# Kernel optimization log

Measured on AMD Instinct MI355X. Metric: run time of the kernel, lower is better.

Reference implementation:

```python
import jax, jax.numpy as jnp
import numpy as np

DECAY = 0.8
CODEBOOK_SIZE = 1024
DIM = 128


def setup_inputs() -> dict:
    key = jax.random.key(0)
    k1, k2 = jax.random.split(key)
    x = jax.random.normal(k1, (16, 4096, DIM), dtype=jnp.float32)
    embed = jax.random.normal(k2, (CODEBOOK_SIZE, DIM), dtype=jnp.float32)
    ema_embed = embed * 1.0  # ema_num_initial = 1.0
    ema_num = jnp.ones((CODEBOOK_SIZE,), dtype=jnp.float32)
    return {"x": x, "embed": embed, "ema_embed": ema_embed, "ema_num": ema_num}


def reference(x, embed, ema_embed, ema_num):
    # flatten: [..., d] -> [N, d]
    shape = x.shape
    flatten = x.reshape(-1, shape[-1])  # [N, d]
    distance = -2.0 * (flatten @ embed.T) + jnp.sum(embed * embed, axis=-1)  # [N, K]
    embed_ind = jnp.argmin(distance, axis=-1)  # [N]
    quantize = embed[embed_ind.reshape(shape[:-1])]  # gather -> [..., d]

    # training branch: onehot^T @ flatten == segment_sum over code indices
    num_curr = jax.ops.segment_sum(
        jnp.ones_like(embed_ind, dtype=jnp.float32), embed_ind,
        num_segments=CODEBOOK_SIZE)  # [K]
    embed_curr = jax.ops.segment_sum(
        flatten.astype(jnp.float32), embed_ind,
        num_segments=CODEBOOK_SIZE)  # [K, d]

    ema_num_new = ema_num * DECAY + (1.0 - DECAY) * num_curr
    ema_embed_new = ema_embed * DECAY + (1.0 - DECAY) * embed_curr
    embed_new = ema_embed_new / ema_num_new[:, None]
    return quantize, embed_new, ema_embed_new, ema_num_new
```

## Files before the change

kernel.cpp:

```cpp
#include <hip/hip_runtime.h>

#define NPTS   65536
#define DIM    128
#define KCODES 1024
#define BM     128
#define TILE_C 32
#define NTHR   256
#define HALF_C 512

typedef short bf16x8 __attribute__((ext_vector_type(8)));
typedef float f32x4  __attribute__((ext_vector_type(4)));

__device__ __forceinline__ short f2bf(float f) {
    unsigned u = __builtin_bit_cast(unsigned, f);
    u = (u + 0x7fffu + ((u >> 16) & 1u)) >> 16;
    return (short)u;
}
__device__ __forceinline__ float bf2f(short s) {
    unsigned u = ((unsigned)(unsigned short)s) << 16;
    return __builtin_bit_cast(float, u);
}
__device__ __forceinline__ void gload_lds16(const void* g, void* l) {
    __builtin_amdgcn_global_load_lds(
        (const __attribute__((address_space(1))) void*)g,
        (__attribute__((address_space(3))) void*)l, 16, 0, 0);
}

__global__ __launch_bounds__(256)
void pack_kernel(const float* __restrict__ embed, short* __restrict__ ebf,
                 int* __restrict__ ghist, int* __restrict__ gcursor,
                 const float* __restrict__ ema_embed,
                 float* __restrict__ acc, float* __restrict__ hn)
{
    __shared__ float partial[256];
    const int t   = threadIdx.x;
    const int b   = blockIdx.x;
    const int g   = b * 256 + t;
    if (g < KCODES) { ghist[g] = 0; gcursor[g] = 0; }
    {
        float4 e = reinterpret_cast<const float4*>(ema_embed)[g];
        float4 o = {0.8f * e.x, 0.8f * e.y, 0.8f * e.z, 0.8f * e.w};
        reinterpret_cast<float4*>(acc)[g] = o;
    }
    const int tc  = g >> 10;
    const int f   = (g >> 6) & 15;
    const int l   = g & 63;
    const int h   = f >> 3;
    const int nt  = (f >> 2) & 1;
    const int akk = f & 3;
    const int hg  = l >> 4;
    const int n   = l & 15;
    const int c   = tc * TILE_C + nt * 16 + n;
    const int d0  = akk * 32 + hg * 8;
    const float* src = embed + (long)c * DIM + d0;
    float4 v0 = *reinterpret_cast<const float4*>(src);
    float4 v1 = *reinterpret_cast<const float4*>(src + 4);
    float vv[8] = {v0.x, v0.y, v0.z, v0.w, v1.x, v1.y, v1.z, v1.w};
    bf16x8 out;
    float ss = 0.f;
    #pragma unroll
    for (int j = 0; j < 8; ++j) {
        short hi = f2bf(vv[j]);
        out[j] = h ? f2bf(vv[j] - bf2f(hi)) : hi;
        ss += vv[j] * vv[j];
    }
    *reinterpret_cast<bf16x8*>(ebf + (long)g * 8) = out;

    if (h == 0) {
        partial[t] = ss;
        __syncthreads();
        if (t < 16) {
            float s = 0.f;
            #pragma unroll
            for (int k = 0; k < 16; ++k) s += partial[t + k * 16];
            hn[tc * TILE_C + nt * 16 + t] = 0.5f * s;
        }
    }
}

__global__ __launch_bounds__(NTHR, 2)
void argmin_kernel(const float* __restrict__ x, const short* __restrict__ ebf,
                   const float* __restrict__ halfnorm, float2* __restrict__ bvbi)
{
    __shared__ short es[2][8192];

    const int t    = threadIdx.x;
    const int lane = t & 63;
    const int w    = t >> 6;
    const int r16  = lane & 15;
    const int h4   = lane >> 4;
    const int half = blockIdx.y;
    const long xbase = (long)blockIdx.x * BM * DIM;
    const int  wp    = w * 32;
    const long sbase = (long)half * 16 * 8192;
    const int  cbase = half * HALF_C;

    bf16x8 ahi[2][4], alo[2][4];
    #pragma unroll
    for (int ms = 0; ms < 2; ++ms) {
        const long prow = xbase + (long)(wp + ms * 16 + r16) * DIM;
        #pragma unroll
        for (int kk = 0; kk < 4; ++kk) {
            const float* s = x + prow + kk * 32 + h4 * 8;
            float4 u0 = *reinterpret_cast<const float4*>(s);
            float4 u1 = *reinterpret_cast<const float4*>(s + 4);
            float vv[8] = {u0.x, u0.y, u0.z, u0.w, u1.x, u1.y, u1.z, u1.w};
            #pragma unroll
            for (int j = 0; j < 8; ++j) {
                short hi = f2bf(vv[j]);
                ahi[ms][kk][j] = hi;
                alo[ms][kk][j] = f2bf(vv[j] - bf2f(hi));
            }
        }
    }

    #pragma unroll
    for (int i = 0; i < 4; ++i) {
        const int f = w * 4 + i;
        gload_lds16(ebf + sbase + f * 512 + lane * 8, &es[0][f * 512]);
    }
    float hnv_cur[2];
    #pragma unroll
    for (int nt = 0; nt < 2; ++nt) hnv_cur[nt] = halfnorm[cbase + nt * 16 + r16];
    __syncthreads();

    float bestv[8];
    int   besti[8];
    #pragma unroll
    for (int s = 0; s < 8; ++s) { bestv[s] = -1e30f; besti[s] = 0; }

    for (int tile = 0; tile < HALF_C / TILE_C; ++tile) {
        float hnv_nxt[2] = {0.f, 0.f};
        if (tile + 1 < HALF_C / TILE_C) {
            const long gbase = sbase + (long)(tile + 1) * 8192;
            #pragma unroll
            for (int i = 0; i < 4; ++i) {
                const int f = w * 4 + i;
                gload_lds16(ebf + gbase + f * 512 + lane * 8, &es[(tile + 1) & 1][f * 512]);
            }
            #pragma unroll
            for (int nt = 0; nt < 2; ++nt)
                hnv_nxt[nt] = halfnorm[cbase + (tile + 1) * TILE_C + nt * 16 + r16];
        }

        const short* buf = es[tile & 1];
        f32x4 C[2][2];
        #pragma unroll
        for (int nt = 0; nt < 2; ++nt)
            #pragma unroll
            for (int ms = 0; ms < 2; ++ms) C[nt][ms] = (f32x4){0.f, 0.f, 0.f, 0.f};

        #pragma unroll
        for (int akk = 0; akk < 4; ++akk) {
            #pragma unroll
            for (int nt = 0; nt < 2; ++nt) {
                bf16x8 Bh = *reinterpret_cast<const bf16x8*>(buf + (nt * 4 + akk) * 512 + lane * 8);
                bf16x8 Bl = *reinterpret_cast<const bf16x8*>(buf + (8 + nt * 4 + akk) * 512 + lane * 8);
                C[nt][0] = __builtin_amdgcn_mfma_f32_16x16x32_bf16(ahi[0][akk], Bh, C[nt][0], 0, 0, 0);
                C[nt][1] = __builtin_amdgcn_mfma_f32_16x16x32_bf16(ahi[1][akk], Bh, C[nt][1], 0, 0, 0);
                C[nt][0] = __builtin_amdgcn_mfma_f32_16x16x32_bf16(alo[0][akk], Bh, C[nt][0], 0, 0, 0);
                C[nt][1] = __builtin_amdgcn_mfma_f32_16x16x32_bf16(alo[1][akk], Bh, C[nt][1], 0, 0, 0);
                C[nt][0] = __builtin_amdgcn_mfma_f32_16x16x32_bf16(ahi[0][akk], Bl, C[nt][0], 0, 0, 0);
                C[nt][1] = __builtin_amdgcn_mfma_f32_16x16x32_bf16(ahi[1][akk], Bl, C[nt][1], 0, 0, 0);
            }
        }

        #pragma unroll
        for (int nt = 0; nt < 2; ++nt) {
            const int c = cbase + tile * TILE_C + nt * 16 + r16;
            #pragma unroll
            for (int ms = 0; ms < 2; ++ms)
                #pragma unroll
                for (int reg = 0; reg < 4; ++reg) {
                    float sc  = C[nt][ms][reg] - hnv_cur[nt];
                    int  slot = ms * 4 + reg;
                    if (sc > bestv[slot]) { bestv[slot] = sc; besti[slot] = c; }
                }
        }
        hnv_cur[0] = hnv_nxt[0];
        hnv_cur[1] = hnv_nxt[1];
        __syncthreads();
    }

    #pragma unroll
    for (int s = 0; s < 8; ++s) {
        float v = bestv[s];
        int   i = besti[s];
        #pragma unroll
        for (int off = 1; off < 16; off <<= 1) {
            float ov = __shfl_xor(v, off);
            int   oi = __shfl_xor(i, off);
            if (ov > v || (ov == v && oi < i)) { v = ov; i = oi; }
        }
        bestv[s] = v; besti[s] = i;
    }
    if (r16 == 0) {
        #pragma unroll
        for (int s = 0; s < 8; ++s) {
            int ms = s >> 2, reg = s & 3;
            int p  = wp + ms * 16 + h4 * 4 + reg;
            bvbi[(long)half * NPTS + blockIdx.x * BM + p] =
                (float2){bestv[s], __int_as_float(besti[s])};
        }
    }
}

__global__ __launch_bounds__(256)
void merge_kernel(const float2* __restrict__ bvbi, const float* __restrict__ embed,
                  int* __restrict__ ind, float* __restrict__ quant,
                  int* __restrict__ ghist)
{
    __shared__ int hist[KCODES];
    __shared__ int bidx[256];
    const int t    = threadIdx.x;
    const int base = blockIdx.x * 256;

    for (int i = t; i < KCODES; i += 256) hist[i] = 0;

    float2 a = bvbi[base + t];
    float2 b = bvbi[NPTS + base + t];
    const int best = (a.x >= b.x) ? __float_as_int(a.y) : __float_as_int(b.y);
    bidx[t] = best;
    ind[base + t] = best;
    __syncthreads();
    atomicAdd(&hist[best], 1);
    __syncthreads();
    for (int i = t; i < KCODES; i += 256)
        if (hist[i]) atomicAdd(&ghist[i], hist[i]);

    float4* dst = reinterpret_cast<float4*>(quant + (long)base * DIM);
    #pragma unroll
    for (int i = 0; i < 32; ++i) {
        int idx = i * 256 + t;
        int p   = idx >> 5;
        int q   = idx & 31;
        int c   = bidx[p];
        dst[idx] = reinterpret_cast<const float4*>(embed + (long)c * DIM)[q];
    }
}

__global__ __launch_bounds__(256)
void scatter_kernel(const int* __restrict__ ghist, const int* __restrict__ ind,
                    const float* __restrict__ ema_num, float* __restrict__ ema_num_new,
                    int* __restrict__ gcursor, int* __restrict__ sorted,
                    int* __restrict__ scode)
{
    __shared__ int off_lds[KCODES];
    __shared__ int wsum[4];
    const int t    = threadIdx.x;
    const int lane = t & 63;
    const int w    = t >> 6;

    int v[4], pre[4];
    int s = 0;
    #pragma unroll
    for (int j = 0; j < 4; ++j) {
        v[j] = ghist[t * 4 + j];
        pre[j] = s;
        s += v[j];
    }
    int incl = s;
    #pragma unroll
    for (int off = 1; off < 64; off <<= 1) {
        int u = __shfl_up(incl, off);
        if (lane >= off) incl += u;
    }
    if (lane == 63) wsum[w] = incl;
    __syncthreads();
    if (t == 0) {
        int a = 0;
        #pragma unroll
        for (int k = 0; k < 4; ++k) { int tmp = wsum[k]; wsum[k] = a; a += tmp; }
    }
    __syncthreads();
    const int excl = wsum[w] + incl - s;
    #pragma unroll
    for (int j = 0; j < 4; ++j) off_lds[t * 4 + j] = excl + pre[j];

    if (blockIdx.x == 0) {
        #pragma unroll
        for (int j = 0; j < 4; ++j)
            ema_num_new[t * 4 + j] = ema_num[t * 4 + j] * 0.8f + 0.2f * (float)v[j];
    }
    __syncthreads();

    const int p = blockIdx.x * 256 + t;
    const int c = ind[p];
    const int pos = off_lds[c] + atomicAdd(&gcursor[c], 1);
    sorted[pos] = p;
    scode[pos]  = c;
}

__global__ __launch_bounds__(128)
void sum2_kernel(const float* __restrict__ x, const int* __restrict__ sorted,
                 const int* __restrict__ scode, float* __restrict__ acc)
{
    __shared__ int sp[64];
    __shared__ int sc[64];
    const int t = threadIdx.x;
    const int base = blockIdx.x * 64;
    if (t < 64) { sp[t] = sorted[base + t]; sc[t] = scode[base + t]; }
    __syncthreads();

    float a = 0.f;
    int cprev = sc[0];
    #pragma unroll 1
    for (int kk = 0; kk < 8; ++kk) {
        float v[8];
        #pragma unroll
        for (int i = 0; i < 8; ++i)
            v[i] = x[(long)sp[kk * 8 + i] * DIM + t];
        #pragma unroll
        for (int i = 0; i < 8; ++i) {
            const int c = sc[kk * 8 + i];
            if (c != cprev) {
                atomicAdd(&acc[(long)cprev * DIM + t], 0.2f * a);
                a = 0.f; cprev = c;
            }
            a += v[i];
        }
    }
    atomicAdd(&acc[(long)cprev * DIM + t], 0.2f * a);
}

__global__ __launch_bounds__(256)
void final_kernel(const float* __restrict__ acc, const float* __restrict__ ema_num_new,
                  float* __restrict__ embed_new)
{
    const int g = blockIdx.x * 256 + threadIdx.x;
    float4 v = reinterpret_cast<const float4*>(acc)[g];
    const float en = ema_num_new[g >> 5];
    float4 o = {v.x / en, v.y / en, v.z / en, v.w / en};
    reinterpret_cast<float4*>(embed_new)[g] = o;
}

extern "C" void kernel_launch(void* const* d_in, const int* in_sizes, int n_in,
                              void* d_out, int out_size, void* d_ws, size_t ws_size,
                              hipStream_t stream)
{
    const float* x         = (const float*)d_in[0];
    const float* embed     = (const float*)d_in[1];
    const float* ema_embed = (const float*)d_in[2];
    const float* ema_num   = (const float*)d_in[3];

    float* out0 = (float*)d_out;
    float* out1 = out0 + 8388608;
    float* out2 = out1 + 131072;
    float* out3 = out2 + 131072;

    char*   ws      = (char*)d_ws;
    float*  hn      = (float*)ws;
    int*    ind     = (int*)(ws + 4096);
    short*  ebf     = (short*)(ws + 266240);
    int*    ghist   = (int*)(ws + 790528);
    int*    gcursor = (int*)(ws + 794624);
    float2* bvbi    = (float2*)(ws + 798720);
    int*    sorted  = (int*)(ws + 798720);
    int*    scode   = (int*)(ws + 1060864);

    pack_kernel<<<128, 256, 0, stream>>>(embed, ebf, ghist, gcursor, ema_embed, out2, hn);
    argmin_kernel<<<dim3(NPTS / BM, 2), NTHR, 0, stream>>>(x, ebf, hn, bvbi);
    merge_kernel<<<NPTS / 256, 256, 0, stream>>>(bvbi, embed, ind, out0, ghist);
    scatter_kernel<<<NPTS / 256, 256, 0, stream>>>(ghist, ind, ema_num, out3,
                                                   gcursor, sorted, scode);
    sum2_kernel<<<NPTS / 64, 128, 0, stream>>>(x, sorted, scode, out2);
    final_kernel<<<128, 256, 0, stream>>>(out2, out3, out1);
}
```

Measured before the change: 116.0 us.

## Load codebook fragments directly from global memory instead of LDS double-buffering

The argmin kernel no longer stages codebook tiles into shared memory with async global-to-LDS loads and barriers. Each wave now reads its bf16 B fragments straight from global memory (through L2/L1), with the tile loop unrolled by four and the occupancy hint raised to three blocks per SM. The aim is to drop the barrier and LDS traffic and let more waves hide latency. In exchange, every wave separately re-reads the same codebook data from cache, which adds global load pressure and latency on the MFMA path.

```diff
diff --git a/kernel.cpp b/kernel.cpp
--- a/kernel.cpp
+++ b/kernel.cpp
@@ -19,11 +19,6 @@
 __device__ __forceinline__ float bf2f(short s) {
     unsigned u = ((unsigned)(unsigned short)s) << 16;
     return __builtin_bit_cast(float, u);
-}
-__device__ __forceinline__ void gload_lds16(const void* g, void* l) {
-    __builtin_amdgcn_global_load_lds(
-        (const __attribute__((address_space(1))) void*)g,
-        (__attribute__((address_space(3))) void*)l, 16, 0, 0);
 }
 
 __global__ __launch_bounds__(256)
@@ -78,12 +73,10 @@
     }
 }
 
-__global__ __launch_bounds__(NTHR, 2)
+__global__ __launch_bounds__(NTHR, 3)
 void argmin_kernel(const float* __restrict__ x, const short* __restrict__ ebf,
                    const float* __restrict__ halfnorm, float2* __restrict__ bvbi)
 {
-    __shared__ short es[2][8192];
-
     const int t    = threadIdx.x;
     const int lane = t & 63;
     const int w    = t >> 6;
@@ -92,8 +85,9 @@
     const int half = blockIdx.y;
     const long xbase = (long)blockIdx.x * BM * DIM;
     const int  wp    = w * 32;
-    const long sbase = (long)half * 16 * 8192;
     const int  cbase = half * HALF_C;
+    const bf16x8* B = reinterpret_cast<const bf16x8*>(
+        ebf + (long)half * 16 * 8192 + lane * 8);
 
     bf16x8 ahi[2][4], alo[2][4];
     #pragma unroll
@@ -114,36 +108,18 @@
         }
     }
 
-    #pragma unroll
-    for (int i = 0; i < 4; ++i) {
-        const int f = w * 4 + i;
-        gload_lds16(ebf + sbase + f * 512 + lane * 8, &es[0][f * 512]);
-    }
-    float hnv_cur[2];
-    #pragma unroll
-    for (int nt = 0; nt < 2; ++nt) hnv_cur[nt] = halfnorm[cbase + nt * 16 + r16];
-    __syncthreads();
-
     float bestv[8];
     int   besti[8];
     #pragma unroll
     for (int s = 0; s < 8; ++s) { bestv[s] = -1e30f; besti[s] = 0; }
 
+    #pragma unroll 4
     for (int tile = 0; tile < HALF_C / TILE_C; ++tile) {
-        float hnv_nxt[2] = {0.f, 0.f};
-        if (tile + 1 < HALF_C / TILE_C) {
-            const long gbase = sbase + (long)(tile + 1) * 8192;
-            #pragma unroll
-            for (int i = 0; i < 4; ++i) {
-                const int f = w * 4 + i;
-                gload_lds16(ebf + gbase + f * 512 + lane * 8, &es[(tile + 1) & 1][f * 512]);
-            }
-            #pragma unroll
-            for (int nt = 0; nt < 2; ++nt)
-                hnv_nxt[nt] = halfnorm[cbase + (tile + 1) * TILE_C + nt * 16 + r16];
-        }
-
-        const short* buf = es[tile & 1];
+        float hnv[2];
+        #pragma unroll
+        for (int nt = 0; nt < 2; ++nt)
+            hnv[nt] = halfnorm[cbase + tile * TILE_C + nt * 16 + r16];
+
         f32x4 C[2][2];
         #pragma unroll
         for (int nt = 0; nt < 2; ++nt)
@@ -154,8 +130,8 @@
         for (int akk = 0; akk < 4; ++akk) {
             #pragma unroll
             for (int nt = 0; nt < 2; ++nt) {
-                bf16x8 Bh = *reinterpret_cast<const bf16x8*>(buf + (nt * 4 + akk) * 512 + lane * 8);
-                bf16x8 Bl = *reinterpret_cast<const bf16x8*>(buf + (8 + nt * 4 + akk) * 512 + lane * 8);
+                bf16x8 Bh = B[(tile * 16 + nt * 4 + akk) * 64];
+                bf16x8 Bl = B[(tile * 16 + 8 + nt * 4 + akk) * 64];
                 C[nt][0] = __builtin_amdgcn_mfma_f32_16x16x32_bf16(ahi[0][akk], Bh, C[nt][0], 0, 0, 0);
                 C[nt][1] = __builtin_amdgcn_mfma_f32_16x16x32_bf16(ahi[1][akk], Bh, C[nt][1], 0, 0, 0);
                 C[nt][0] = __builtin_amdgcn_mfma_f32_16x16x32_bf16(alo[0][akk], Bh, C[nt][0], 0, 0, 0);
@@ -172,14 +148,11 @@
             for (int ms = 0; ms < 2; ++ms)
                 #pragma unroll
                 for (int reg = 0; reg < 4; ++reg) {
-                    float sc  = C[nt][ms][reg] - hnv_cur[nt];
+                    float sc  = C[nt][ms][reg] - hnv[nt];
                     int  slot = ms * 4 + reg;
                     if (sc > bestv[slot]) { bestv[slot] = sc; besti[slot] = c; }
                 }
         }
-        hnv_cur[0] = hnv_nxt[0];
-        hnv_cur[1] = hnv_nxt[1];
-        __syncthreads();
     }
 
     #pragma unroll
```

Measured after the change: 153.4 us. 32.3% more time.

## Triple-buffer codebook tiles in LDS with explicit vmcnt waits

Applied to the files above, without the earlier changes.

Grows the LDS codebook staging from two to three buffers so each tile is prefetched two iterations ahead. The full __syncthreads is replaced by raw s_barrier plus hand-written s_waitcnt vmcnt counts, so a wave waits only for the tile it is about to use. The goal is to hide global-to-LDS load latency behind the MFMA work. In exchange, LDS per block grows, which may reduce occupancy, and the vmcnt counts are fragile because the halfnorm loads are also counted.

```diff
diff --git a/kernel.cpp b/kernel.cpp
--- a/kernel.cpp
+++ b/kernel.cpp
@@ -7,6 +7,7 @@
 #define TILE_C 32
 #define NTHR   256
 #define HALF_C 512
+#define NTILE  (HALF_C / TILE_C)
 
 typedef short bf16x8 __attribute__((ext_vector_type(8)));
 typedef float f32x4  __attribute__((ext_vector_type(4)));
@@ -82,7 +83,7 @@
 void argmin_kernel(const float* __restrict__ x, const short* __restrict__ ebf,
                    const float* __restrict__ halfnorm, float2* __restrict__ bvbi)
 {
-    __shared__ short es[2][8192];
+    __shared__ short es[3][8192];
 
     const int t    = threadIdx.x;
     const int lane = t & 63;
@@ -92,8 +93,8 @@
     const int half = blockIdx.y;
     const long xbase = (long)blockIdx.x * BM * DIM;
     const int  wp    = w * 32;
-    const long sbase = (long)half * 16 * 8192;
     const int  cbase = half * HALF_C;
+    const short* eb  = ebf + (long)half * 16 * 8192;
 
     bf16x8 ahi[2][4], alo[2][4];
     #pragma unroll
@@ -117,33 +118,48 @@
     #pragma unroll
     for (int i = 0; i < 4; ++i) {
         const int f = w * 4 + i;
-        gload_lds16(ebf + sbase + f * 512 + lane * 8, &es[0][f * 512]);
-    }
-    float hnv_cur[2];
+        gload_lds16(eb + (long)f * 512 + lane * 8, &es[0][f * 512]);
+    }
+    #pragma unroll
+    for (int i = 0; i < 4; ++i) {
+        const int f = w * 4 + i;
+        gload_lds16(eb + (long)8192 + f * 512 + lane * 8, &es[1][f * 512]);
+    }
+    float hnv_cur[2], hnv_nxt[2];
     #pragma unroll
     for (int nt = 0; nt < 2; ++nt) hnv_cur[nt] = halfnorm[cbase + nt * 16 + r16];
-    __syncthreads();
 
     float bestv[8];
     int   besti[8];
     #pragma unroll
     for (int s = 0; s < 8; ++s) { bestv[s] = -1e30f; besti[s] = 0; }
 
-    for (int tile = 0; tile < HALF_C / TILE_C; ++tile) {
-        float hnv_nxt[2] = {0.f, 0.f};
-        if (tile + 1 < HALF_C / TILE_C) {
-            const long gbase = sbase + (long)(tile + 1) * 8192;
+    int ia = 0, ic = 2;
+
+    #pragma unroll 1
+    for (int tile = 0; tile < NTILE; ++tile) {
+        __builtin_amdgcn_s_barrier();
+
+        if (tile + 2 < NTILE) {
+            const long gbase = (long)(tile + 2) * 8192;
             #pragma unroll
             for (int i = 0; i < 4; ++i) {
                 const int f = w * 4 + i;
-                gload_lds16(ebf + gbase + f * 512 + lane * 8, &es[(tile + 1) & 1][f * 512]);
+                gload_lds16(eb + gbase + f * 512 + lane * 8, &es[ic][f * 512]);
             }
+        }
+        if (tile + 1 < NTILE) {
             #pragma unroll
             for (int nt = 0; nt < 2; ++nt)
                 hnv_nxt[nt] = halfnorm[cbase + (tile + 1) * TILE_C + nt * 16 + r16];
         }
 
-        const short* buf = es[tile & 1];
+        if (tile < NTILE - 2)       asm volatile("s_waitcnt vmcnt(6)" ::: "memory");
+        else if (tile == NTILE - 2) asm volatile("s_waitcnt vmcnt(2)" ::: "memory");
+        else                        asm volatile("s_waitcnt vmcnt(0)" ::: "memory");
+
+        __builtin_amdgcn_s_barrier();
+
         f32x4 C[2][2];
         #pragma unroll
         for (int nt = 0; nt < 2; ++nt)
@@ -154,8 +170,8 @@
         for (int akk = 0; akk < 4; ++akk) {
             #pragma unroll
             for (int nt = 0; nt < 2; ++nt) {
-                bf16x8 Bh = *reinterpret_cast<const bf16x8*>(buf + (nt * 4 + akk) * 512 + lane * 8);
-                bf16x8 Bl = *reinterpret_cast<const bf16x8*>(buf + (8 + nt * 4 + akk) * 512 + lane * 8);
+                bf16x8 Bh = *reinterpret_cast<const bf16x8*>(&es[ia][(nt * 4 + akk) * 512 + lane * 8]);
+                bf16x8 Bl = *reinterpret_cast<const bf16x8*>(&es[ia][(8 + nt * 4 + akk) * 512 + lane * 8]);
                 C[nt][0] = __builtin_amdgcn_mfma_f32_16x16x32_bf16(ahi[0][akk], Bh, C[nt][0], 0, 0, 0);
                 C[nt][1] = __builtin_amdgcn_mfma_f32_16x16x32_bf16(ahi[1][akk], Bh, C[nt][1], 0, 0, 0);
                 C[nt][0] = __builtin_amdgcn_mfma_f32_16x16x32_bf16(alo[0][akk], Bh, C[nt][0], 0, 0, 0);
@@ -179,7 +195,10 @@
         }
         hnv_cur[0] = hnv_nxt[0];
         hnv_cur[1] = hnv_nxt[1];
-        __syncthreads();
+        int tmp = ia;
+        ia = (ia + 1) % 3;
+        ic = (ic + 1) % 3;
+        (void)tmp;
     }
 
     #pragma unroll
```

Result: no change. 115.5 us (-0.4%).

## Use single-pass fp16 MFMA for distances and merge quarter argmins via atomicMax

Applied to the files above, without the earlier changes.

Replaces the three-pass bf16 hi/lo split matmul with a single fp16 MFMA pass, cutting MFMA work to a third, and stores the codebook and its norms in fp16-rounded form. The codebook is split into four quarters across blockIdx.y with 64-code tiles and higher occupancy. Per-quarter results are combined through a 64-bit packed atomicMax key (monotone float bits, inverted index for tie-break), which replaces the two-half buffer compare in merge. The risk is that fp16 precision flips argmin choices for near-tied codes compared with the fp32-accurate reference, and fp16 overflow is possible for large inputs.

```diff
diff --git a/kernel.cpp b/kernel.cpp
--- a/kernel.cpp
+++ b/kernel.cpp
@@ -1,52 +1,53 @@
 #include <hip/hip_runtime.h>
 
-#define NPTS   65536
-#define DIM    128
-#define KCODES 1024
-#define BM     128
-#define TILE_C 32
-#define NTHR   256
-#define HALF_C 512
-
-typedef short bf16x8 __attribute__((ext_vector_type(8)));
-typedef float f32x4  __attribute__((ext_vector_type(4)));
-
-__device__ __forceinline__ short f2bf(float f) {
-    unsigned u = __builtin_bit_cast(unsigned, f);
-    u = (u + 0x7fffu + ((u >> 16) & 1u)) >> 16;
-    return (short)u;
-}
-__device__ __forceinline__ float bf2f(short s) {
-    unsigned u = ((unsigned)(unsigned short)s) << 16;
-    return __builtin_bit_cast(float, u);
-}
+#define NPTS    65536
+#define DIM     128
+#define KCODES  1024
+#define BM      128
+#define TILE_C  64
+#define NTHR    256
+#define QUART_C 256
+#define NTILE   (QUART_C / TILE_C)
+
+typedef _Float16 f16x8 __attribute__((ext_vector_type(8)));
+typedef float    f32x4 __attribute__((ext_vector_type(4)));
+
 __device__ __forceinline__ void gload_lds16(const void* g, void* l) {
     __builtin_amdgcn_global_load_lds(
         (const __attribute__((address_space(1))) void*)g,
         (__attribute__((address_space(3))) void*)l, 16, 0, 0);
 }
+__device__ __forceinline__ unsigned mono32(float f) {
+    unsigned u = __builtin_bit_cast(unsigned, f);
+    return (u & 0x80000000u) ? ~u : (u | 0x80000000u);
+}
 
 __global__ __launch_bounds__(256)
-void pack_kernel(const float* __restrict__ embed, short* __restrict__ ebf,
+void pack_kernel(const float* __restrict__ embed, _Float16* __restrict__ ebf,
                  int* __restrict__ ghist, int* __restrict__ gcursor,
-                 const float* __restrict__ ema_embed,
-                 float* __restrict__ acc, float* __restrict__ hn)
+                 const float* __restrict__ ema_embed, float* __restrict__ acc,
+                 float* __restrict__ hn, unsigned long long* __restrict__ kmax)
 {
     __shared__ float partial[256];
-    const int t   = threadIdx.x;
-    const int b   = blockIdx.x;
-    const int g   = b * 256 + t;
+    const int t = threadIdx.x;
+    const int b = blockIdx.x;
+    const int g = b * 256 + t;
     if (g < KCODES) { ghist[g] = 0; gcursor[g] = 0; }
     {
-        float4 e = reinterpret_cast<const float4*>(ema_embed)[g];
-        float4 o = {0.8f * e.x, 0.8f * e.y, 0.8f * e.z, 0.8f * e.w};
-        reinterpret_cast<float4*>(acc)[g] = o;
-    }
+        float4 e0 = reinterpret_cast<const float4*>(ema_embed)[g];
+        float4 e1 = reinterpret_cast<const float4*>(ema_embed)[g + 16384];
+        reinterpret_cast<float4*>(acc)[g] =
+            (float4){0.8f * e0.x, 0.8f * e0.y, 0.8f * e0.z, 0.8f * e0.w};
+        reinterpret_cast<float4*>(acc)[g + 16384] =
+            (float4){0.8f * e1.x, 0.8f * e1.y, 0.8f * e1.z, 0.8f * e1.w};
+    }
+    #pragma unroll
+    for (int k = 0; k < 4; ++k) kmax[g * 4 + k] = 0ull;
+
     const int tc  = g >> 10;
     const int f   = (g >> 6) & 15;
     const int l   = g & 63;
-    const int h   = f >> 3;
-    const int nt  = (f >> 2) & 1;
+    const int nt  = f >> 2;
     const int akk = f & 3;
     const int hg  = l >> 4;
     const int n   = l & 15;
@@ -56,72 +57,68 @@
     float4 v0 = *reinterpret_cast<const float4*>(src);
     float4 v1 = *reinterpret_cast<const float4*>(src + 4);
     float vv[8] = {v0.x, v0.y, v0.z, v0.w, v1.x, v1.y, v1.z, v1.w};
-    bf16x8 out;
+    f16x8 out;
     float ss = 0.f;
     #pragma unroll
     for (int j = 0; j < 8; ++j) {
-        short hi = f2bf(vv[j]);
-        out[j] = h ? f2bf(vv[j] - bf2f(hi)) : hi;
-        ss += vv[j] * vv[j];
-    }
-    *reinterpret_cast<bf16x8*>(ebf + (long)g * 8) = out;
-
-    if (h == 0) {
-        partial[t] = ss;
-        __syncthreads();
-        if (t < 16) {
-            float s = 0.f;
-            #pragma unroll
-            for (int k = 0; k < 16; ++k) s += partial[t + k * 16];
-            hn[tc * TILE_C + nt * 16 + t] = 0.5f * s;
-        }
-    }
-}
-
-__global__ __launch_bounds__(NTHR, 2)
-void argmin_kernel(const float* __restrict__ x, const short* __restrict__ ebf,
-                   const float* __restrict__ halfnorm, float2* __restrict__ bvbi)
-{
-    __shared__ short es[2][8192];
-
-    const int t    = threadIdx.x;
-    const int lane = t & 63;
-    const int w    = t >> 6;
-    const int r16  = lane & 15;
-    const int h4   = lane >> 4;
-    const int half = blockIdx.y;
+        _Float16 h = (_Float16)vv[j];
+        out[j] = h;
+        float r = (float)h;
+        ss += r * r;
+    }
+    *reinterpret_cast<f16x8*>(ebf + (long)g * 8) = out;
+
+    partial[t] = ss;
+    __syncthreads();
+    if (t < 16) {
+        float s = 0.f;
+        #pragma unroll
+        for (int k = 0; k < 16; ++k) s += partial[t + k * 16];
+        hn[(b >> 2) * TILE_C + (b & 3) * 16 + t] = 0.5f * s;
+    }
+}
+
+__global__ __launch_bounds__(NTHR, 4)
+void argmin_kernel(const float* __restrict__ x, const _Float16* __restrict__ ebf,
+                   const float* __restrict__ halfnorm,
+                   unsigned long long* __restrict__ kmax)
+{
+    __shared__ _Float16 es[2][8192];
+
+    const int t     = threadIdx.x;
+    const int lane  = t & 63;
+    const int w     = t >> 6;
+    const int r16   = lane & 15;
+    const int h4    = lane >> 4;
+    const int quart = blockIdx.y;
     const long xbase = (long)blockIdx.x * BM * DIM;
     const int  wp    = w * 32;
-    const long sbase = (long)half * 16 * 8192;
-    const int  cbase = half * HALF_C;
-
-    bf16x8 ahi[2][4], alo[2][4];
+    const int  qbase = quart * QUART_C;
+    const _Float16* eb = ebf + (long)quart * QUART_C * DIM;
+
+    f16x8 a[2][4];
     #pragma unroll
     for (int ms = 0; ms < 2; ++ms) {
         const long prow = xbase + (long)(wp + ms * 16 + r16) * DIM;
         #pragma unroll
-        for (int kk = 0; kk < 4; ++kk) {
-            const float* s = x + prow + kk * 32 + h4 * 8;
+        for (int akk = 0; akk < 4; ++akk) {
+            const float* s = x + prow + akk * 32 + h4 * 8;
             float4 u0 = *reinterpret_cast<const float4*>(s);
             float4 u1 = *reinterpret_cast<const float4*>(s + 4);
             float vv[8] = {u0.x, u0.y, u0.z, u0.w, u1.x, u1.y, u1.z, u1.w};
             #pragma unroll
-            for (int j = 0; j < 8; ++j) {
-                short hi = f2bf(vv[j]);
-                ahi[ms][kk][j] = hi;
-                alo[ms][kk][j] = f2bf(vv[j] - bf2f(hi));
-            }
+            for (int j = 0; j < 8; ++j) a[ms][akk][j] = (_Float16)vv[j];
         }
     }
 
     #pragma unroll
     for (int i = 0; i < 4; ++i) {
         const int f = w * 4 + i;
-        gload_lds16(ebf + sbase + f * 512 + lane * 8, &es[0][f * 512]);
-    }
-    float hnv_cur[2];
-    #pragma unroll
-    for (int nt = 0; nt < 2; ++nt) hnv_cur[nt] = halfnorm[cbase + nt * 16 + r16];
+        gload_lds16(eb + (long)f * 512 + lane * 8, &es[0][f * 512]);
+    }
+    float hnv_cur[4], hnv_nxt[4];
+    #pragma unroll
+    for (int nt = 0; nt < 4; ++nt) hnv_cur[nt] = halfnorm[qbase + nt * 16 + r16];
     __syncthreads();
 
     float bestv[8];
@@ -129,45 +126,40 @@
     #pragma unroll
     for (int s = 0; s < 8; ++s) { bestv[s] = -1e30f; besti[s] = 0; }
 
-    for (int tile = 0; tile < HALF_C / TILE_C; ++tile) {
-        float hnv_nxt[2] = {0.f, 0.f};
-        if (tile + 1 < HALF_C / TILE_C) {
-            const long gbase = sbase + (long)(tile + 1) * 8192;
+    #pragma unroll 1
+    for (int tile = 0; tile < NTILE; ++tile) {
+        if (tile + 1 < NTILE) {
+            const long gbase = (long)(tile + 1) * 8192;
             #pragma unroll
             for (int i = 0; i < 4; ++i) {
                 const int f = w * 4 + i;
-                gload_lds16(ebf + gbase + f * 512 + lane * 8, &es[(tile + 1) & 1][f * 512]);
+                gload_lds16(eb + gbase + f * 512 + lane * 8, &es[(tile + 1) & 1][f * 512]);
             }
             #pragma unroll
-            for (int nt = 0; nt < 2; ++nt)
-                hnv_nxt[nt] = halfnorm[cbase + (tile + 1) * TILE_C + nt * 16 + r16];
-        }
-
-        const short* buf = es[tile & 1];
-        f32x4 C[2][2];
-        #pragma unroll
-        for (int nt = 0; nt < 2; ++nt)
+            for (int nt = 0; nt < 4; ++nt)
+                hnv_nxt[nt] = halfnorm[qbase + (tile + 1) * TILE_C + nt * 16 + r16];
+        }
+
+        f32x4 C[4][2];
+        #pragma unroll
+        for (int nt = 0; nt < 4; ++nt)
             #pragma unroll
             for (int ms = 0; ms < 2; ++ms) C[nt][ms] = (f32x4){0.f, 0.f, 0.f, 0.f};
 
         #pragma unroll
         for (int akk = 0; akk < 4; ++akk) {
             #pragma unroll
-            for (int nt = 0; nt < 2; ++nt) {
-                bf16x8 Bh = *reinterpret_cast<const bf16x8*>(buf + (nt * 4 + akk) * 512 + lane * 8);
-                bf16x8 Bl = *reinterpret_cast<const bf16x8*>(buf + (8 + nt * 4 + akk) * 512 + lane * 8);
-                C[nt][0] = __builtin_amdgcn_mfma_f32_16x16x32_bf16(ahi[0][akk], Bh, C[nt][0], 0, 0, 0);
-                C[nt][1] = __builtin_amdgcn_mfma_f32_16x16x32_bf16(ahi[1][akk], Bh, C[nt][1], 0, 0, 0);
-                C[nt][0] = __builtin_amdgcn_mfma_f32_16x16x32_bf16(alo[0][akk], Bh, C[nt][0], 0, 0, 0);
-                C[nt][1] = __builtin_amdgcn_mfma_f32_16x16x32_bf16(alo[1][akk], Bh, C[nt][1], 0, 0, 0);
-                C[nt][0] = __builtin_amdgcn_mfma_f32_16x16x32_bf16(ahi[0][akk], Bl, C[nt][0], 0, 0, 0);
-                C[nt][1] = __builtin_amdgcn_mfma_f32_16x16x32_bf16(ahi[1][akk], Bl, C[nt][1], 0, 0, 0);
+            for (int nt = 0; nt < 4; ++nt) {
+                f16x8 B = *reinterpret_cast<const f16x8*>(
+                    &es[tile & 1][(nt * 4 + akk) * 512 + lane * 8]);
+                C[nt][0] = __builtin_amdgcn_mfma_f32_16x16x32_f16(a[0][akk], B, C[nt][0], 0, 0, 0);
+                C[nt][1] = __builtin_amdgcn_mfma_f32_16x16x32_f16(a[1][akk], B, C[nt][1], 0, 0, 0);
             }
         }
 
         #pragma unroll
-        for (int nt = 0; nt < 2; ++nt) {
-            const int c = cbase + tile * TILE_C + nt * 16 + r16;
+        for (int nt = 0; nt < 4; ++nt) {
+            const int c = qbase + tile * TILE_C + nt * 16 + r16;
             #pragma unroll
             for (int ms = 0; ms < 2; ++ms)
                 #pragma unroll
@@ -177,8 +169,8 @@
                     if (sc > bestv[slot]) { bestv[slot] = sc; besti[slot] = c; }
                 }
         }
-        hnv_cur[0] = hnv_nxt[0];
-        hnv_cur[1] = hnv_nxt[1];
+        #pragma unroll
+        for (int nt = 0; nt < 4; ++nt) hnv_cur[nt] = hnv_nxt[nt];
         __syncthreads();
     }
 
@@ -199,16 +191,18 @@
         for (int s = 0; s < 8; ++s) {
             int ms = s >> 2, reg = s & 3;
             int p  = wp + ms * 16 + h4 * 4 + reg;
-            bvbi[(long)half * NPTS + blockIdx.x * BM + p] =
-                (float2){bestv[s], __int_as_float(besti[s])};
+            unsigned long long key =
+                ((unsigned long long)mono32(bestv[s]) << 32) |
+                (unsigned long long)(0x3FFu - (unsigned)besti[s]);
+            atomicMax(&kmax[blockIdx.x * BM + p], key);
         }
     }
 }
 
 __global__ __launch_bounds__(256)
-void merge_kernel(const float2* __restrict__ bvbi, const float* __restrict__ embed,
-                  int* __restrict__ ind, float* __restrict__ quant,
-                  int* __restrict__ ghist)
+void merge_kernel(const unsigned long long* __restrict__ kmax,
+                  const float* __restrict__ embed, int* __restrict__ ind,
+                  float* __restrict__ quant, int* __restrict__ ghist)
 {
     __shared__ int hist[KCODES];
     __shared__ int bidx[256];
@@ -217,9 +211,8 @@
 
     for (int i = t; i < KCODES; i += 256) hist[i] = 0;
 
-    float2 a = bvbi[base + t];
-    float2 b = bvbi[NPTS + base + t];
-    const int best = (a.x >= b.x) ? __float_as_int(a.y) : __float_as_int(b.y);
+    const unsigned long long k = kmax[base + t];
+    const int best = 0x3FF - (int)(k & 0x3FFu);
     bidx[t] = best;
     ind[base + t] = best;
     __syncthreads();
@@ -348,19 +341,20 @@
     float* out2 = out1 + 131072;
     float* out3 = out2 + 131072;
 
-    char*   ws      = (char*)d_ws;
-    float*  hn      = (float*)ws;
-    int*    ind     = (int*)(ws + 4096);
-    short*  ebf     = (short*)(ws + 266240);
-    int*    ghist   = (int*)(ws + 790528);
-    int*    gcursor = (int*)(ws + 794624);
-    float2* bvbi    = (float2*)(ws + 798720);
-    int*    sorted  = (int*)(ws + 798720);
-    int*    scode   = (int*)(ws + 1060864);
-
-    pack_kernel<<<128, 256, 0, stream>>>(embed, ebf, ghist, gcursor, ema_embed, out2, hn);
-    argmin_kernel<<<dim3(NPTS / BM, 2), NTHR, 0, stream>>>(x, ebf, hn, bvbi);
-    merge_kernel<<<NPTS / 256, 256, 0, stream>>>(bvbi, embed, ind, out0, ghist);
+    char* ws = (char*)d_ws;
+    float*              hn      = (float*)ws;
+    int*                ind     = (int*)(ws + 4096);
+    _Float16*           ebf     = (_Float16*)(ws + 266240);
+    int*                ghist   = (int*)(ws + 528384);
+    int*                gcursor = (int*)(ws + 532480);
+    unsigned long long* kmax    = (unsigned long long*)(ws + 536576);
+    int*                sorted  = (int*)(ws + 536576);
+    int*                scode   = (int*)(ws + 798720);
+
+    pack_kernel<<<64, 256, 0, stream>>>(embed, ebf, ghist, gcursor, ema_embed,
+                                        out2, hn, kmax);
+    argmin_kernel<<<dim3(NPTS / BM, 4), NTHR, 0, stream>>>(x, ebf, hn, kmax);
+    merge_kernel<<<NPTS / 256, 256, 0, stream>>>(kmax, embed, ind, out0, ghist);
     scatter_kernel<<<NPTS / 256, 256, 0, stream>>>(ghist, ind, ema_num, out3,
                                                    gcursor, sorted, scode);
     sum2_kernel<<<NPTS / 64, 128, 0, stream>>>(x, sorted, scode, out2);
```

Result: faster. 100.3 us (-13.5%).
